# Performance work log

Hardware: AMD Instinct MI355X
Metric: run time of the kernel (lower is better)

The kernel has to match this reference:

```python
import jax, jax.numpy as jnp
import numpy as np
from jax import lax

MARGIN = 0.5
EPS = 1e-12


def _l2norm(x, axis=-1):
    n = jnp.sqrt(jnp.sum(x * x, axis=axis, keepdims=True))
    return x / jnp.maximum(n, EPS)


def setup_inputs() -> dict:
    key = jax.random.key(0)
    ks = jax.random.split(key, 18)
    B, T, N, Din = 1, 8, 4096, 128
    hid = 256
    D = 2 * hid  # out_dim = 2*hidden_dim[-1]
    Tp, Ttr, M, K = 4, 5, 2048, 16
    s = 0.05
    return {
        "x_feature": jax.random.normal(ks[0], (B, Ttr, N, 1), jnp.float32),
        "x_graph": jax.random.normal(ks[1], (B, T, N, Din), jnp.float32),
        "x_graph_inv": jax.random.normal(ks[2], (B, T, N, Din), jnp.float32),
        "temp_y": jax.random.randint(ks[3], (Tp, M, 2 + K), 0, N),
        "is_leaf": jax.random.uniform(ks[4], (Tp, N), dtype=jnp.float32),
        "W_gcn": jax.random.normal(ks[5], (Din, hid), jnp.float32) * s,
        "b_gcn": jnp.zeros((hid,), jnp.float32),
        "Wx_zr": jax.random.normal(ks[6], (D, 2 * D), jnp.float32) * s,
        "Wh_zr": jax.random.normal(ks[7], (D, 2 * D), jnp.float32) * s,
        "b_zr": jnp.zeros((2 * D,), jnp.float32),
        "Wx_c": jax.random.normal(ks[8], (D, D), jnp.float32) * s,
        "Wh_c": jax.random.normal(ks[9], (D, D), jnp.float32) * s,
        "b_c": jnp.zeros((D,), jnp.float32),
        "h_vecs": jax.random.normal(ks[10], (Tp, D), jnp.float32),
        "W_leaf": jax.random.normal(ks[11], (D, 1), jnp.float32) * s,
        "b_leaf": jnp.zeros((1,), jnp.float32),
        "W_conv": jax.random.normal(ks[12], (Ttr, Tp), jnp.float32) * s,
        "b_conv": jnp.zeros((Tp,), jnp.float32),
        "cur_node_num": N,
    }


def reference(x_feature, x_graph, x_graph_inv, temp_y, is_leaf,
              W_gcn, b_gcn, Wx_zr, Wh_zr, b_zr, Wx_c, Wh_c, b_c,
              h_vecs, W_leaf, b_leaf, W_conv, b_conv, cur_node_num):
    B = x_graph.shape[0]
    N_all = x_graph.shape[2]
    # t_gcn on both graph views, concat -> [B,T,N,D]
    h = jax.nn.relu(jnp.einsum('btnd,dh->btnh', x_graph, W_gcn) + b_gcn)
    h_inv = jax.nn.relu(jnp.einsum('btnd,dh->btnh', x_graph_inv, W_gcn) + b_gcn)
    h_final = jnp.concatenate((h, h_inv), axis=-1)
    D = h_final.shape[-1]

    # sequential GRU (TGCNCell) over time_span via scan
    def cell(hs, x):
        zr = jax.nn.sigmoid(x @ Wx_zr + hs @ Wh_zr + b_zr)
        z, r = jnp.split(zr, 2, axis=-1)
        c = jnp.tanh(x @ Wx_c + (r * hs) @ Wh_c + b_c)
        return z * hs + (1.0 - z) * c, None

    h0 = jnp.zeros((B, N_all, D), h_final.dtype)
    hT, _ = lax.scan(cell, h0, jnp.moveaxis(h_final, 1, 0))
    h_trans = _l2norm(hT.reshape(-1, D)[:cur_node_num])  # [N,D]

    # grid predictions (t_conv surrogate): [B,Ttr,N,1] -> [Tp, B*N] -> [Tp,N]
    feat = x_feature[..., 0].transpose(0, 2, 1)            # [B,N,Ttr]
    g = feat @ W_conv + b_conv                             # [B,N,Tp]
    grid_x = jnp.moveaxis(g, 2, 0).reshape(g.shape[-1], -1)[:, :cur_node_num]

    # Householder reflections per predicted step
    hn = _l2norm(h_vecs)                                   # [Tp,D]
    W_trans = jnp.eye(D, dtype=hn.dtype) - 2.0 * hn[:, :, None] * hn[:, None, :]

    leaf_logits = jax.nn.sigmoid(h_trans @ W_leaf + b_leaf)  # [N,1]
    lvec = leaf_logits[:, 0]

    def per_t(W_t, idx_t, yleaf_t, grid_t):
        pos = h_trans[idx_t[:, 1]]            # [M,D]
        neg = h_trans[idx_t[:, 2:]]           # [M,K,D]
        a = pos @ W_t                          # [M,D]
        score_neg = 1.0 - jnp.einsum('md,mkd->mk', a, neg)
        score_pos = 1.0 - jnp.sum(a * pos, axis=-1, keepdims=True)
        loss_off = jnp.mean(jax.nn.relu(score_pos - score_neg + MARGIN))
        # BCEWithLogits applied to sigmoid outputs (faithful to source)
        loss_leaf = jnp.mean(jnp.maximum(lvec, 0.0) - lvec * yleaf_t + jnp.log1p(jnp.exp(-jnp.abs(lvec))))
        h_s = h_trans @ W_t                    # [N,D]
        score_all = h_s @ h_s.T                # [N,N]
        final = lvec * grid_t                  # [N]
        att = score_all @ final                # [N]
        return att, loss_off, loss_leaf

    att_pre, lo, ll = jax.vmap(per_t)(W_trans, temp_y, is_leaf, grid_x)
    return att_pre, jnp.mean(lo), jnp.mean(ll)
```

## Files before the change

### kernel.cpp

```cpp
#include <hip/hip_runtime.h>
#include <hip/hip_bf16.h>
#include <hip/hip_fp16.h>
#include <math.h>

typedef __hip_bfloat16 bf16;
typedef __attribute__((ext_vector_type(8))) short short8;
typedef __attribute__((ext_vector_type(4))) float f32x4;

union UB { short8 v; bf16 e[8]; };
union UH { short8 v; __half e[8]; };

__device__ __forceinline__ float wred(float v) {
  #pragma unroll
  for (int o = 32; o > 0; o >>= 1) v += __shfl_xor(v, o, 64);
  return v;
}
__device__ __forceinline__ float sigf(float x) { return 1.f / (1.f + expf(-x)); }

__device__ __forceinline__ float sig2(float x) {
  return __builtin_amdgcn_rcpf(1.f + exp2f(-1.44269504f * x));
}
__device__ __forceinline__ float tanh2(float x) {
  float ax = fminf(fabsf(x), 30.f);
  float e = exp2f(2.88539008f * ax);
  float r = 1.f - 2.f * __builtin_amdgcn_rcpf(e + 1.f);
  return copysignf(r, x);
}

__device__ __forceinline__ void gl_lds16(const bf16* g, const bf16* lds) {
  __builtin_amdgcn_global_load_lds((const __attribute__((address_space(1))) void*)g,
                                   (__attribute__((address_space(3))) void*)lds,
                                   16, 0, 0);
}
__device__ __forceinline__ void gl_lds16c(const bf16* g, const bf16* lds) {
  __builtin_amdgcn_global_load_lds((const __attribute__((address_space(1))) void*)g,
                                   (__attribute__((address_space(3))) void*)lds,
                                   16, 0, 1);
}
__device__ __forceinline__ f32x4 mfma16(short8 a, short8 b, f32x4 c) {
  return __builtin_amdgcn_mfma_f32_16x16x32_bf16(a, b, c, 0, 0, 0);
}

__device__ __forceinline__ void gang_sync(unsigned* f) {
  __syncthreads();
  if (threadIdx.x == 0) {
    __hip_atomic_fetch_add(f, 1u, __ATOMIC_RELAXED, __HIP_MEMORY_SCOPE_AGENT);
    int it = 0;
    while (__hip_atomic_load(f, __ATOMIC_RELAXED, __HIP_MEMORY_SCOPE_AGENT) < 4u) {
      __builtin_amdgcn_s_sleep(2);
      if (++it > (1 << 27)) break;
    }
  }
  __syncthreads();
  asm volatile("" ::: "memory");
}

__global__ __launch_bounds__(256, 2)
void gemmx(const bf16* __restrict__ A, const bf16* __restrict__ Wxzrt,
           const bf16* __restrict__ Wxct, const float* __restrict__ b_zr,
           const float* __restrict__ b_c, bf16* __restrict__ xzrp,
           bf16* __restrict__ xcp)
{
  __shared__ __align__(16) char smem[34816];
  bf16* As = (bf16*)smem;
  bf16* Bs = (bf16*)(smem + 16384);
  __half* Ts = (__half*)smem;

  const int tid  = threadIdx.x;
  const int wave = tid >> 6, lane = tid & 63;
  const int lm = lane & 15, q = lane >> 4;
  const int brow = blockIdx.x, bcol = blockIdx.y;
  const int wr = (wave >> 1) * 64, wc = (wave & 1) * 64;
  const int srow = lane >> 3, sslot = lane & 7;

  const bf16* Bt; const float* bias; bf16* C; int ldc, colbase;
  if (bcol < 8) { Bt = Wxzrt + (size_t)bcol * 128 * 512; bias = b_zr; C = xzrp; ldc = 1024; colbase = bcol * 128; }
  else          { Bt = Wxct + (size_t)(bcol - 8) * 128 * 512; bias = b_c; C = xcp; ldc = 512; colbase = (bcol - 8) * 128; }

  f32x4 acc[4][4];
  #pragma unroll
  for (int i = 0; i < 4; ++i)
    #pragma unroll
    for (int j = 0; j < 4; ++j) acc[i][j] = (f32x4){0.f, 0.f, 0.f, 0.f};

  for (int kb = 0; kb < 512; kb += 64) {
    #pragma unroll
    for (int j = 0; j < 4; ++j) {
      int ml = wave * 32 + j * 8 + srow;
      int cg = sslot ^ (ml & 7);
      gl_lds16(A + (size_t)(brow * 128 + ml) * 512 + kb + cg * 8, As + (wave * 4 + j) * 512);
      gl_lds16(Bt + (size_t)ml * 512 + kb + cg * 8, Bs + (wave * 4 + j) * 512);
    }
    __syncthreads();
    #pragma unroll
    for (int ks = 0; ks < 2; ++ks) {
      short8 af[4], bfr[4];
      #pragma unroll
      for (int i = 0; i < 4; ++i) {
        int cg = ks * 4 + q;
        int ml = wr + i * 16 + lm;
        af[i]  = *(const short8*)(As + ml * 64 + ((cg ^ (ml & 7)) * 8));
        int nl = wc + i * 16 + lm;
        bfr[i] = *(const short8*)(Bs + nl * 64 + ((cg ^ (nl & 7)) * 8));
      }
      #pragma unroll
      for (int i = 0; i < 4; ++i)
        #pragma unroll
        for (int j = 0; j < 4; ++j)
          acc[i][j] = mfma16(af[i], bfr[j], acc[i][j]);
    }
    __syncthreads();
  }
  #pragma unroll
  for (int i = 0; i < 4; ++i)
    #pragma unroll
    for (int j = 0; j < 4; ++j) {
      int col = wc + j * 16 + lm;
      float bv = bias[colbase + col];
      #pragma unroll
      for (int p = 0; p < 4; ++p)
        Ts[(wr + i * 16 + q * 4 + p) * 136 + col] = __float2half(acc[i][j][p] + bv);
    }
  __syncthreads();
  int rg = tid >> 4, cl = tid & 15;
  #pragma unroll
  for (int v = 0; v < 8; ++v) {
    int row = v * 16 + rg;
    UH t; t.v = *(const short8*)(Ts + row * 136 + cl * 8);
    UB o;
    #pragma unroll
    for (int e = 0; e < 8; ++e) o.e[e] = __float2bfloat16(__half2float(t.e[e]));
    *(short8*)(C + (size_t)(brow * 128 + row) * ldc + colbase + cl * 8) = o.v;
  }
}

__global__ __launch_bounds__(256, 2)
void gcnk(const float* __restrict__ Ag, const float* __restrict__ Agi,
          const bf16* __restrict__ Wgt, const float* __restrict__ bias,
          bf16* __restrict__ out)
{
  __shared__ __align__(16) char smem[34816];
  bf16* As = (bf16*)smem;
  bf16* Bs = (bf16*)(smem + 16384);
  __half* Ts = (__half*)smem;

  const int tid  = threadIdx.x;
  const int wave = tid >> 6, lane = tid & 63;
  const int lm = lane & 15, q = lane >> 4;
  const int brow = blockIdx.x, bcol = blockIdx.y;
  const int z = blockIdx.z, cout = z * 256;
  const float* A = z ? Agi : Ag;
  const int wr = (wave >> 1) * 64, wc = (wave & 1) * 64;
  const int srow = lane >> 3, sslot = lane & 7;

  f32x4 acc[4][4];
  #pragma unroll
  for (int i = 0; i < 4; ++i)
    #pragma unroll
    for (int j = 0; j < 4; ++j) acc[i][j] = (f32x4){0.f, 0.f, 0.f, 0.f};

  for (int kb = 0; kb < 128; kb += 64) {
    #pragma unroll
    for (int j = 0; j < 4; ++j) {
      int ml = wave * 32 + j * 8 + srow;
      int cg = sslot ^ (ml & 7);
      const float* src = A + (size_t)(brow * 128 + ml) * 128 + kb + cg * 8;
      bf16 tmp[8];
      #pragma unroll
      for (int e = 0; e < 8; ++e) tmp[e] = __float2bfloat16(src[e]);
      *(short8*)(As + ml * 64 + sslot * 8) = *(const short8*)tmp;
      gl_lds16(Wgt + (size_t)(bcol * 128 + ml) * 128 + kb + cg * 8,
               Bs + (wave * 4 + j) * 512);
    }
    __syncthreads();
    #pragma unroll
    for (int ks = 0; ks < 2; ++ks) {
      short8 af[4], bfr[4];
      #pragma unroll
      for (int i = 0; i < 4; ++i) {
        int cg = ks * 4 + q;
        int ml = wr + i * 16 + lm;
        af[i]  = *(const short8*)(As + ml * 64 + ((cg ^ (ml & 7)) * 8));
        int nl = wc + i * 16 + lm;
        bfr[i] = *(const short8*)(Bs + nl * 64 + ((cg ^ (nl & 7)) * 8));
      }
      #pragma unroll
      for (int i = 0; i < 4; ++i)
        #pragma unroll
        for (int j = 0; j < 4; ++j)
          acc[i][j] = mfma16(af[i], bfr[j], acc[i][j]);
    }
    __syncthreads();
  }
  #pragma unroll
  for (int i = 0; i < 4; ++i)
    #pragma unroll
    for (int j = 0; j < 4; ++j) {
      int col = wc + j * 16 + lm;
      float bv = bias[bcol * 128 + col];
      #pragma unroll
      for (int p = 0; p < 4; ++p)
        Ts[(wr + i * 16 + q * 4 + p) * 136 + col] = __float2half(acc[i][j][p] + bv);
    }
  __syncthreads();
  int rg = tid >> 4, cl = tid & 15;
  #pragma unroll
  for (int v = 0; v < 8; ++v) {
    int row = v * 16 + rg;
    UH t; t.v = *(const short8*)(Ts + row * 136 + cl * 8);
    UB o;
    #pragma unroll
    for (int e = 0; e < 8; ++e) o.e[e] = __float2bfloat16(fmaxf(__half2float(t.e[e]), 0.f));
    *(short8*)(out + (size_t)(brow * 128 + row) * 512 + cout + bcol * 128 + cl * 8) = o.v;
  }
}

__global__ __launch_bounds__(512, 1)
void grup(const bf16* __restrict__ Wzr, const bf16* __restrict__ Wc,
          const bf16* __restrict__ xzrp, const bf16* __restrict__ xcp,
          bf16* __restrict__ rhb, bf16* __restrict__ hsb,
          unsigned* __restrict__ flags)
{
  __shared__ __align__(16) bf16   As[64 * 512];
  __shared__ __align__(16) __half zs[64 * 128];
  __shared__ __align__(16) bf16   hs[64 * 128];
  __half* Ts = (__half*)As;

  const int tid  = threadIdx.x;
  const int w    = tid >> 6, lane = tid & 63;
  const int lm   = lane & 15, q = lane >> 4;
  const int bid  = blockIdx.x;
  const int s    = (bid >> 3) & 3;
  const int g    = ((bid >> 5) << 3) | (bid & 7);
  const int grow = g * 64;
  const int grp  = w >> 2, wq = w & 3;
  const int rh_  = w & 1, cq = w >> 1;
  const int prow = tid >> 3;
  const size_t gr = (size_t)(grow + prow);
  const int pc1 = (tid & 7) * 32;
  const int pc2 = (tid & 7) * 16;
  unsigned* gf = flags + g * 16;

  for (int t = 0; t < 8; ++t) {
    const bool t0 = (t == 0);
    const bf16* xz = xzrp + (size_t)t * 4096 * 1024;
    const bf16* xc = xcp  + (size_t)t * 4096 * 512;

    {
      const bool zchunk = (pc1 < 128);
      const int zrcol = zchunk ? (s * 128 + pc1) : (512 + s * 128 + pc1 - 128);
      UB xv[4];
      #pragma unroll
      for (int j = 0; j < 4; ++j)
        xv[j].v = *(const short8*)(xz + gr * 1024 + zrcol + j * 8);

      f32x4 acc[4][2];
      #pragma unroll
      for (int mf = 0; mf < 4; ++mf)
        #pragma unroll
        for (int nf = 0; nf < 2; ++nf) acc[mf][nf] = (f32x4){0.f, 0.f, 0.f, 0.f};

      if (!t0) {
        #pragma unroll
        for (int j = 0; j < 8; ++j) {
          int row = w * 8 + j;
          gl_lds16c(hsb + (size_t)(grow + row) * 512 + ((lane ^ (row & 7)) * 8),
                    As + row * 512);
        }
        __syncthreads();

        const int nb0 = (grp ? 32 : 0) + s * 8 + wq * 2;
        const bf16* Bp = Wzr + (size_t)nb0 * 8192 + lane * 8;
        #pragma unroll
        for (int KS = 0; KS < 16; ++KS) {
          short8 a[4], b[2];
          #pragma unroll
          for (int mf = 0; mf < 4; ++mf) {
            int row = mf * 16 + lm;
            a[mf] = *(const short8*)(As + row * 512 + (((KS * 4 + q) ^ (row & 7)) * 8));
          }
          #pragma unroll
          for (int nf = 0; nf < 2; ++nf)
            b[nf] = *(const short8*)(Bp + (size_t)nf * 8192 + KS * 512);
          #pragma unroll
          for (int nf = 0; nf < 2; ++nf)
            #pragma unroll
            for (int mf = 0; mf < 4; ++mf)
              acc[mf][nf] = mfma16(a[mf], b[nf], acc[mf][nf]);
        }
        __syncthreads();
      }

      #pragma unroll
      for (int mf = 0; mf < 4; ++mf)
        #pragma unroll
        for (int nf = 0; nf < 2; ++nf)
          #pragma unroll
          for (int p = 0; p < 4; ++p)
            Ts[(mf * 16 + q * 4 + p) * 264 + w * 32 + nf * 16 + lm] =
              __float2half(acc[mf][nf][p]);
      __syncthreads();

      #pragma unroll
      for (int j = 0; j < 4; ++j) {
        int c = pc1 + j * 8;
        UH tv; tv.v = *(const short8*)(Ts + prow * 264 + c);
        if (zchunk) {
          UH o;
          #pragma unroll
          for (int e = 0; e < 8; ++e)
            o.e[e] = __float2half(sig2(__half2float(tv.e[e]) + (float)xv[j].e[e]));
          *(short8*)(zs + prow * 128 + c) = o.v;
        } else if (!t0) {
          UB h8; h8.v = *(const short8*)(hs + prow * 128 + (c - 128));
          UB o;
          #pragma unroll
          for (int e = 0; e < 8; ++e) {
            float r = sig2(__half2float(tv.e[e]) + (float)xv[j].e[e]);
            o.e[e] = __float2bfloat16(r * (float)h8.e[e]);
          }
          *(short8*)(rhb + gr * 512 + s * 128 + (c - 128)) = o.v;
        }
      }
    }
    gang_sync(gf + 2 * t);

    {
      UB xv[2];
      #pragma unroll
      for (int j = 0; j < 2; ++j)
        xv[j].v = *(const short8*)(xc + gr * 512 + s * 128 + pc2 + j * 8);

      f32x4 acc[2][2];
      #pragma unroll
      for (int mf = 0; mf < 2; ++mf)
        #pragma unroll
        for (int nf = 0; nf < 2; ++nf) acc[mf][nf] = (f32x4){0.f, 0.f, 0.f, 0.f};

      if (!t0) {
        #pragma unroll
        for (int j = 0; j < 8; ++j) {
          int row = w * 8 + j;
          gl_lds16c(rhb + (size_t)(grow + row) * 512 + ((lane ^ (row & 7)) * 8),
                    As + row * 512);
        }
        __syncthreads();

        const bf16* Bp = Wc + (size_t)(s * 8 + cq * 2) * 8192 + lane * 8;
        #pragma unroll
        for (int KS = 0; KS < 16; ++KS) {
          short8 a[2], b[2];
          #pragma unroll
          for (int mf = 0; mf < 2; ++mf) {
            int row = rh_ * 32 + mf * 16 + lm;
            a[mf] = *(const short8*)(As + row * 512 + (((KS * 4 + q) ^ (row & 7)) * 8));
          }
          #pragma unroll
          for (int nf = 0; nf < 2; ++nf)
            b[nf] = *(const short8*)(Bp + (size_t)nf * 8192 + KS * 512);
          #pragma unroll
          for (int nf = 0; nf < 2; ++nf)
            #pragma unroll
            for (int mf = 0; mf < 2; ++mf)
              acc[mf][nf] = mfma16(a[mf], b[nf], acc[mf][nf]);
        }
        __syncthreads();
      }

      #pragma unroll
      for (int mf = 0; mf < 2; ++mf)
        #pragma unroll
        for (int nf = 0; nf < 2; ++nf)
          #pragma unroll
          for (int p = 0; p < 4; ++p)
            Ts[(rh_ * 32 + mf * 16 + q * 4 + p) * 136 + cq * 32 + nf * 16 + lm] =
              __float2half(acc[mf][nf][p]);
      __syncthreads();

      #pragma unroll
      for (int j = 0; j < 2; ++j) {
        int c = pc2 + j * 8;
        UH tv; tv.v = *(const short8*)(Ts + prow * 136 + c);
        UH zv; zv.v = *(const short8*)(zs + prow * 128 + c);
        UB h8;
        if (!t0) h8.v = *(const short8*)(hs + prow * 128 + c);
        UB o;
        #pragma unroll
        for (int e = 0; e < 8; ++e) {
          float cd = tanh2(__half2float(tv.e[e]) + (float)xv[j].e[e]);
          float zc = __half2float(zv.e[e]);
          float ho = t0 ? 0.f : (float)h8.e[e];
          o.e[e] = __float2bfloat16(zc * ho + (1.f - zc) * cd);
        }
        *(short8*)(hs + prow * 128 + c) = o.v;
        *(short8*)(hsb + gr * 512 + s * 128 + c) = o.v;
      }
    }
    if (t < 7) gang_sync(gf + 2 * t + 1);
  }
}

__global__ void prep(const float* __restrict__ Wh_zr, const float* __restrict__ Wh_c,
                     const float* __restrict__ Wx_zr, const float* __restrict__ Wx_c,
                     const float* __restrict__ W_gcn,
                     bf16* __restrict__ Whzrt, bf16* __restrict__ Whct,
                     bf16* __restrict__ Wxzrt, bf16* __restrict__ Wxct,
                     bf16* __restrict__ Wgt) {
  int i = blockIdx.x * 256 + threadIdx.x;
  if (i < 524288) {
    int n = i >> 9, k = i & 511;
    int off = ((n >> 4) * 16 + (k >> 5)) * 512 + ((k >> 3) & 3) * 128 + (n & 15) * 8 + (k & 7);
    Whzrt[off] = __float2bfloat16(Wh_zr[(size_t)k * 1024 + n]);
  } else if (i < 786432) {
    int j = i - 524288; int n = j >> 9, k = j & 511;
    int off = ((n >> 4) * 16 + (k >> 5)) * 512 + ((k >> 3) & 3) * 128 + (n & 15) * 8 + (k & 7);
    Whct[off] = __float2bfloat16(Wh_c[(size_t)k * 512 + n]);
  } else if (i < 1310720) {
    int j = i - 786432; int n = j >> 9, k = j & 511;
    Wxzrt[j] = __float2bfloat16(Wx_zr[(size_t)k * 1024 + n]);
  } else if (i < 1572864) {
    int j = i - 1310720; int n = j >> 9, k = j & 511;
    Wxct[j] = __float2bfloat16(Wx_c[(size_t)k * 512 + n]);
  } else {
    int j = i - 1572864; int n = j >> 7, k = j & 127;
    Wgt[j] = __float2bfloat16(W_gcn[(size_t)k * 256 + n]);
  }
}

__global__ void norm_lvec(const bf16* __restrict__ hsb, const float* __restrict__ Wl,
                          const float* __restrict__ bl, const float* __restrict__ hv,
                          bf16* __restrict__ Htrb, float* __restrict__ lv,
                          float* __restrict__ hn) {
  int w = threadIdx.x >> 6, lane = threadIdx.x & 63;
  if (blockIdx.x == 1024) {
    float x[8], ss = 0.f;
    #pragma unroll
    for (int j = 0; j < 8; ++j) { x[j] = hv[w * 512 + lane * 8 + j]; ss += x[j] * x[j]; }
    ss = wred(ss);
    float inv = 1.f / fmaxf(sqrtf(ss), 1e-12f);
    #pragma unroll
    for (int j = 0; j < 8; ++j) hn[w * 512 + lane * 8 + j] = x[j] * inv;
    return;
  }
  int n = blockIdx.x * 4 + w;
  float x[8], ss = 0.f;
  #pragma unroll
  for (int j = 0; j < 8; ++j) {
    x[j] = (float)hsb[(size_t)n * 512 + lane * 8 + j];
    ss += x[j] * x[j];
  }
  ss = wred(ss);
  float inv = 1.f / fmaxf(sqrtf(ss), 1e-12f);
  float dot = 0.f;
  #pragma unroll
  for (int j = 0; j < 8; ++j) {
    float vv = x[j] * inv;
    Htrb[(size_t)n * 512 + lane * 8 + j] = __float2bfloat16(vv);
    dot += vv * Wl[lane * 8 + j];
  }
  dot = wred(dot);
  if (lane == 0) lv[n] = sigf(dot + bl[0]);
}

__global__ void htf(const bf16* __restrict__ Htrb, const float* __restrict__ xf,
                    const float* __restrict__ Wc, const float* __restrict__ bc,
                    const float* __restrict__ lv, float* __restrict__ v) {
  __shared__ float fin_s[4][64];
  int ch = blockIdx.x;
  int d = threadIdx.x;
  int n0 = ch * 64;
  if (d < 256) {
    int t = d >> 6, i = d & 63, n = n0 + i;
    float g = bc[t];
    #pragma unroll
    for (int tt = 0; tt < 5; ++tt) g += xf[tt * 4096 + n] * Wc[tt * 4 + t];
    fin_s[t][i] = lv[n] * g;
  }
  __syncthreads();
  float s0 = 0.f, s1 = 0.f, s2 = 0.f, s3 = 0.f;
  for (int i = 0; i < 64; ++i) {
    float hv = (float)Htrb[(size_t)(n0 + i) * 512 + d];
    s0 += hv * fin_s[0][i];
    s1 += hv * fin_s[1][i];
    s2 += hv * fin_s[2][i];
    s3 += hv * fin_s[3][i];
  }
  atomicAdd(&v[d], s0);
  atomicAdd(&v[512 + d], s1);
  atomicAdd(&v[1024 + d], s2);
  atomicAdd(&v[1536 + d], s3);
}

__global__ void attk(const bf16* __restrict__ Htrb, const float* __restrict__ v,
                     float* __restrict__ out) {
  int w = threadIdx.x >> 6, lane = threadIdx.x & 63;
  int n = blockIdx.x * 4 + w;
  float x[8];
  #pragma unroll
  for (int j = 0; j < 8; ++j) x[j] = (float)Htrb[(size_t)n * 512 + lane * 8 + j];
  #pragma unroll
  for (int t = 0; t < 4; ++t) {
    float s = 0.f;
    #pragma unroll
    for (int j = 0; j < 8; ++j) s += x[j] * v[t * 512 + lane * 8 + j];
    s = wred(s);
    if (lane == 0) out[t * 4096 + n] = s;
  }
}

__global__ void loff(const bf16* __restrict__ Htrb, const float* __restrict__ hn,
                     const int* __restrict__ ty, float* __restrict__ loffp) {
  int w = threadIdx.x >> 6, lane = threadIdx.x & 63;
  int t = blockIdx.y;
  int m = blockIdx.x * 4 + w;
  const int* row = ty + ((size_t)t * 2048 + m) * 18;
  int pi = row[1];
  float p[8], hv[8], c = 0.f;
  #pragma unroll
  for (int j = 0; j < 8; ++j) {
    p[j]  = (float)Htrb[(size_t)pi * 512 + lane * 8 + j];
    hv[j] = hn[t * 512 + lane * 8 + j];
    c += p[j] * hv[j];
  }
  c = wred(c);
  float a[8], sp = 0.f;
  #pragma unroll
  for (int j = 0; j < 8; ++j) { a[j] = p[j] - 2.f * c * hv[j]; sp += a[j] * p[j]; }
  sp = wred(sp);
  float acc = 0.f;
  for (int k = 0; k < 16; ++k) {
    int ni = row[2 + k];
    float sn = 0.f;
    #pragma unroll
    for (int j = 0; j < 8; ++j) sn += a[j] * (float)Htrb[(size_t)ni * 512 + lane * 8 + j];
    sn = wred(sn);
    acc += fmaxf(sn - sp + 0.5f, 0.f);
  }
  __shared__ float sbuf[4];
  if (lane == 0) sbuf[w] = acc;
  __syncthreads();
  if (threadIdx.x == 0)
    loffp[t * 512 + blockIdx.x] = sbuf[0] + sbuf[1] + sbuf[2] + sbuf[3];
}

__global__ void fini(const float* __restrict__ loffp, const float* __restrict__ lv,
                     const float* __restrict__ yl, float* __restrict__ out) {
  int tid = threadIdx.x, w = tid >> 6, lane = tid & 63;
  float s = 0.f, s2 = 0.f;
  for (int i = tid; i < 2048; i += 256) s += loffp[i];
  for (int i = tid; i < 4096; i += 256) {
    float l = lv[i];
    float ym = 0.25f * (yl[i] + yl[4096 + i] + yl[8192 + i] + yl[12288 + i]);
    s2 += fmaxf(l, 0.f) - l * ym + log1pf(expf(-fabsf(l)));
  }
  s = wred(s); s2 = wred(s2);
  __shared__ float sb[4], sb2[4];
  if (lane == 0) { sb[w] = s; sb2[w] = s2; }
  __syncthreads();
  if (tid == 0) {
    out[16384] = (sb[0] + sb[1] + sb[2] + sb[3]) / (4.f * 2048.f * 16.f);
    out[16385] = (sb2[0] + sb2[1] + sb2[2] + sb2[3]) / 4096.f;
  }
}

__global__ void wsprobe(float marker, float* out) {
  if (threadIdx.x == 0) out[0] = marker;
}

extern "C" void kernel_launch(void* const* d_in, const int* in_sizes, int n_in,
                              void* d_out, int out_size, void* d_ws, size_t ws_size,
                              hipStream_t stream) {
  const float* x_feature   = (const float*)d_in[0];
  const float* x_graph     = (const float*)d_in[1];
  const float* x_graph_inv = (const float*)d_in[2];
  const int*   temp_y      = (const int*)d_in[3];
  const float* is_leaf     = (const float*)d_in[4];
  const float* W_gcn       = (const float*)d_in[5];
  const float* b_gcn       = (const float*)d_in[6];
  const float* Wx_zr       = (const float*)d_in[7];
  const float* Wh_zr       = (const float*)d_in[8];
  const float* b_zr        = (const float*)d_in[9];
  const float* Wx_c        = (const float*)d_in[10];
  const float* Wh_c        = (const float*)d_in[11];
  const float* b_c         = (const float*)d_in[12];
  const float* h_vecs      = (const float*)d_in[13];
  const float* W_leaf      = (const float*)d_in[14];
  const float* b_leaf      = (const float*)d_in[15];
  const float* W_conv      = (const float*)d_in[16];
  const float* b_conv      = (const float*)d_in[17];
  float* out = (float*)d_out;
  (void)in_sizes; (void)n_in; (void)out_size;

  const size_t NEED = 156000000;
  if (ws_size < NEED) {
    wsprobe<<<1, 64, 0, stream>>>(1000.f + (float)(ws_size >> 20), out);
    return;
  }

  char* ws = (char*)d_ws;
  size_t off = 0;
  auto alloc = [&](size_t bytes) -> void* {
    void* p = ws + off;
    off = (off + bytes + 255) & ~(size_t)255;
    return p;
  };
  bf16*   Whzrt = (bf16*)  alloc((size_t)1024 * 512 * 2);
  bf16*   Whct  = (bf16*)  alloc((size_t)512 * 512 * 2);
  bf16*   Wxzrt = (bf16*)  alloc((size_t)1024 * 512 * 2);
  bf16*   Wxct  = (bf16*)  alloc((size_t)512 * 512 * 2);
  bf16*   Wgt   = (bf16*)  alloc((size_t)256 * 128 * 2);
  bf16*   hfin  = (bf16*)  alloc((size_t)32768 * 512 * 2);
  bf16*   xzrp  = (bf16*)  alloc((size_t)32768 * 1024 * 2);
  bf16*   xcp   = (bf16*)  alloc((size_t)32768 * 512 * 2);
  bf16*   hsb   = (bf16*)  alloc((size_t)4096 * 512 * 2);
  bf16*   rhb   = (bf16*)  alloc((size_t)4096 * 512 * 2);
  float*  lv    = (float*) alloc(4096 * 4);
  float*  hn    = (float*) alloc(4 * 512 * 4);
  float*  v     = (float*) alloc(4 * 512 * 4);
  float*  loffp = (float*) alloc(2048 * 4);
  unsigned* flags = (unsigned*)alloc(64 * 16 * 4);
  bf16*   Htrb  = hfin;

  hipMemsetAsync(v, 0, 4 * 512 * 4, stream);
  hipMemsetAsync(flags, 0, 64 * 16 * 4, stream);

  prep<<<6272, 256, 0, stream>>>(Wh_zr, Wh_c, Wx_zr, Wx_c, W_gcn,
                                 Whzrt, Whct, Wxzrt, Wxct, Wgt);
  gcnk<<<dim3(256, 2, 2), 256, 0, stream>>>(x_graph, x_graph_inv, Wgt, b_gcn, hfin);
  gemmx<<<dim3(256, 12), 256, 0, stream>>>(hfin, Wxzrt, Wxct, b_zr, b_c, xzrp, xcp);

  grup<<<256, 512, 0, stream>>>(Whzrt, Whct, xzrp, xcp, rhb, hsb, flags);

  norm_lvec<<<1025, 256, 0, stream>>>(hsb, W_leaf, b_leaf, h_vecs, Htrb, lv, hn);
  htf<<<64, 512, 0, stream>>>(Htrb, x_feature, W_conv, b_conv, lv, v);
  attk<<<1024, 256, 0, stream>>>(Htrb, v, out);
  loff<<<dim3(512, 4), 256, 0, stream>>>(Htrb, hn, temp_y, loffp);
  fini<<<1, 256, 0, stream>>>(loffp, lv, is_leaf, out);
}
```

Before: 448.4 us.

## Fuse input-projection GEMM into persistent GRU kernel, dropping xzrp/xcp buffers

Removes the separate gemmx kernel that precomputed x@Wx_zr and x@Wx_c for all timesteps into large bf16 buffers. The persistent GRU kernel now loads each timestep's hfin rows into a new shared-memory tile and does the input-projection MFMAs alongside the hidden-state ones, with biases folded into the accumulator initialisation. This saves the intermediate writes and reads and one launch. In exchange it puts more MFMA work and shared memory on the serial recurrent critical path, where only 256 blocks run.

New measurement: 665.7 us. 48.5% more time.

```diff
diff --git a/kernel.cpp b/kernel.cpp
--- a/kernel.cpp
+++ b/kernel.cpp
@@ -56,85 +56,6 @@
 }
 
 __global__ __launch_bounds__(256, 2)
-void gemmx(const bf16* __restrict__ A, const bf16* __restrict__ Wxzrt,
-           const bf16* __restrict__ Wxct, const float* __restrict__ b_zr,
-           const float* __restrict__ b_c, bf16* __restrict__ xzrp,
-           bf16* __restrict__ xcp)
-{
-  __shared__ __align__(16) char smem[34816];
-  bf16* As = (bf16*)smem;
-  bf16* Bs = (bf16*)(smem + 16384);
-  __half* Ts = (__half*)smem;
-
-  const int tid  = threadIdx.x;
-  const int wave = tid >> 6, lane = tid & 63;
-  const int lm = lane & 15, q = lane >> 4;
-  const int brow = blockIdx.x, bcol = blockIdx.y;
-  const int wr = (wave >> 1) * 64, wc = (wave & 1) * 64;
-  const int srow = lane >> 3, sslot = lane & 7;
-
-  const bf16* Bt; const float* bias; bf16* C; int ldc, colbase;
-  if (bcol < 8) { Bt = Wxzrt + (size_t)bcol * 128 * 512; bias = b_zr; C = xzrp; ldc = 1024; colbase = bcol * 128; }
-  else          { Bt = Wxct + (size_t)(bcol - 8) * 128 * 512; bias = b_c; C = xcp; ldc = 512; colbase = (bcol - 8) * 128; }
-
-  f32x4 acc[4][4];
-  #pragma unroll
-  for (int i = 0; i < 4; ++i)
-    #pragma unroll
-    for (int j = 0; j < 4; ++j) acc[i][j] = (f32x4){0.f, 0.f, 0.f, 0.f};
-
-  for (int kb = 0; kb < 512; kb += 64) {
-    #pragma unroll
-    for (int j = 0; j < 4; ++j) {
-      int ml = wave * 32 + j * 8 + srow;
-      int cg = sslot ^ (ml & 7);
-      gl_lds16(A + (size_t)(brow * 128 + ml) * 512 + kb + cg * 8, As + (wave * 4 + j) * 512);
-      gl_lds16(Bt + (size_t)ml * 512 + kb + cg * 8, Bs + (wave * 4 + j) * 512);
-    }
-    __syncthreads();
-    #pragma unroll
-    for (int ks = 0; ks < 2; ++ks) {
-      short8 af[4], bfr[4];
-      #pragma unroll
-      for (int i = 0; i < 4; ++i) {
-        int cg = ks * 4 + q;
-        int ml = wr + i * 16 + lm;
-        af[i]  = *(const short8*)(As + ml * 64 + ((cg ^ (ml & 7)) * 8));
-        int nl = wc + i * 16 + lm;
-        bfr[i] = *(const short8*)(Bs + nl * 64 + ((cg ^ (nl & 7)) * 8));
-      }
-      #pragma unroll
-      for (int i = 0; i < 4; ++i)
-        #pragma unroll
-        for (int j = 0; j < 4; ++j)
-          acc[i][j] = mfma16(af[i], bfr[j], acc[i][j]);
-    }
-    __syncthreads();
-  }
-  #pragma unroll
-  for (int i = 0; i < 4; ++i)
-    #pragma unroll
-    for (int j = 0; j < 4; ++j) {
-      int col = wc + j * 16 + lm;
-      float bv = bias[colbase + col];
-      #pragma unroll
-      for (int p = 0; p < 4; ++p)
-        Ts[(wr + i * 16 + q * 4 + p) * 136 + col] = __float2half(acc[i][j][p] + bv);
-    }
-  __syncthreads();
-  int rg = tid >> 4, cl = tid & 15;
-  #pragma unroll
-  for (int v = 0; v < 8; ++v) {
-    int row = v * 16 + rg;
-    UH t; t.v = *(const short8*)(Ts + row * 136 + cl * 8);
-    UB o;
-    #pragma unroll
-    for (int e = 0; e < 8; ++e) o.e[e] = __float2bfloat16(__half2float(t.e[e]));
-    *(short8*)(C + (size_t)(brow * 128 + row) * ldc + colbase + cl * 8) = o.v;
-  }
-}
-
-__global__ __launch_bounds__(256, 2)
 void gcnk(const float* __restrict__ Ag, const float* __restrict__ Agi,
           const bf16* __restrict__ Wgt, const float* __restrict__ bias,
           bf16* __restrict__ out)
@@ -217,11 +138,13 @@
 
 __global__ __launch_bounds__(512, 1)
 void grup(const bf16* __restrict__ Wzr, const bf16* __restrict__ Wc,
-          const bf16* __restrict__ xzrp, const bf16* __restrict__ xcp,
-          bf16* __restrict__ rhb, bf16* __restrict__ hsb,
-          unsigned* __restrict__ flags)
+          const bf16* __restrict__ Wxzr, const bf16* __restrict__ Wxc,
+          const bf16* __restrict__ hfin, const float* __restrict__ bzr,
+          const float* __restrict__ bc, bf16* __restrict__ rhb,
+          bf16* __restrict__ hsb, unsigned* __restrict__ flags)
 {
   __shared__ __align__(16) bf16   As[64 * 512];
+  __shared__ __align__(16) bf16   Xs[64 * 512];
   __shared__ __align__(16) __half zs[64 * 128];
   __shared__ __align__(16) bf16   hs[64 * 128];
   __half* Ts = (__half*)As;
@@ -243,23 +166,15 @@
 
   for (int t = 0; t < 8; ++t) {
     const bool t0 = (t == 0);
-    const bf16* xz = xzrp + (size_t)t * 4096 * 1024;
-    const bf16* xc = xcp  + (size_t)t * 4096 * 512;
 
     {
-      const bool zchunk = (pc1 < 128);
-      const int zrcol = zchunk ? (s * 128 + pc1) : (512 + s * 128 + pc1 - 128);
-      UB xv[4];
-      #pragma unroll
-      for (int j = 0; j < 4; ++j)
-        xv[j].v = *(const short8*)(xz + gr * 1024 + zrcol + j * 8);
-
-      f32x4 acc[4][2];
-      #pragma unroll
-      for (int mf = 0; mf < 4; ++mf)
-        #pragma unroll
-        for (int nf = 0; nf < 2; ++nf) acc[mf][nf] = (f32x4){0.f, 0.f, 0.f, 0.f};
-
+      const bf16* xsrc = hfin + ((size_t)(t * 4096) + grow) * 512;
+      #pragma unroll
+      for (int j = 0; j < 8; ++j) {
+        int row = w * 8 + j;
+        gl_lds16(xsrc + (size_t)row * 512 + ((lane ^ (row & 7)) * 8),
+                 Xs + row * 512);
+      }
       if (!t0) {
         #pragma unroll
         for (int j = 0; j < 8; ++j) {
@@ -267,9 +182,20 @@
           gl_lds16c(hsb + (size_t)(grow + row) * 512 + ((lane ^ (row & 7)) * 8),
                     As + row * 512);
         }
-        __syncthreads();
-
-        const int nb0 = (grp ? 32 : 0) + s * 8 + wq * 2;
+      }
+      __syncthreads();
+
+      const int nb0 = (grp ? 32 : 0) + s * 8 + wq * 2;
+      f32x4 acc[4][2];
+      #pragma unroll
+      for (int nf = 0; nf < 2; ++nf) {
+        float bv = bzr[(nb0 + nf) * 16 + lm];
+        #pragma unroll
+        for (int mf = 0; mf < 4; ++mf)
+          acc[mf][nf] = (f32x4){bv, bv, bv, bv};
+      }
+
+      if (!t0) {
         const bf16* Bp = Wzr + (size_t)nb0 * 8192 + lane * 8;
         #pragma unroll
         for (int KS = 0; KS < 16; ++KS) {
@@ -288,8 +214,28 @@
             for (int mf = 0; mf < 4; ++mf)
               acc[mf][nf] = mfma16(a[mf], b[nf], acc[mf][nf]);
         }
-        __syncthreads();
-      }
+      }
+      {
+        const bf16* Bp = Wxzr + (size_t)nb0 * 8192 + lane * 8;
+        #pragma unroll
+        for (int KS = 0; KS < 16; ++KS) {
+          short8 a[4], b[2];
+          #pragma unroll
+          for (int mf = 0; mf < 4; ++mf) {
+            int row = mf * 16 + lm;
+            a[mf] = *(const short8*)(Xs + row * 512 + (((KS * 4 + q) ^ (row & 7)) * 8));
+          }
+          #pragma unroll
+          for (int nf = 0; nf < 2; ++nf)
+            b[nf] = *(const short8*)(Bp + (size_t)nf * 8192 + KS * 512);
+          #pragma unroll
+          for (int nf = 0; nf < 2; ++nf)
+            #pragma unroll
+            for (int mf = 0; mf < 4; ++mf)
+              acc[mf][nf] = mfma16(a[mf], b[nf], acc[mf][nf]);
+        }
+      }
+      __syncthreads();
 
       #pragma unroll
       for (int mf = 0; mf < 4; ++mf)
@@ -305,18 +251,18 @@
       for (int j = 0; j < 4; ++j) {
         int c = pc1 + j * 8;
         UH tv; tv.v = *(const short8*)(Ts + prow * 264 + c);
-        if (zchunk) {
+        if (c < 128) {
           UH o;
           #pragma unroll
           for (int e = 0; e < 8; ++e)
-            o.e[e] = __float2half(sig2(__half2float(tv.e[e]) + (float)xv[j].e[e]));
+            o.e[e] = __float2half(sig2(__half2float(tv.e[e])));
           *(short8*)(zs + prow * 128 + c) = o.v;
         } else if (!t0) {
           UB h8; h8.v = *(const short8*)(hs + prow * 128 + (c - 128));
           UB o;
           #pragma unroll
           for (int e = 0; e < 8; ++e) {
-            float r = sig2(__half2float(tv.e[e]) + (float)xv[j].e[e]);
+            float r = sig2(__half2float(tv.e[e]));
             o.e[e] = __float2bfloat16(r * (float)h8.e[e]);
           }
           *(short8*)(rhb + gr * 512 + s * 128 + (c - 128)) = o.v;
@@ -326,17 +272,6 @@
     gang_sync(gf + 2 * t);
 
     {
-      UB xv[2];
-      #pragma unroll
-      for (int j = 0; j < 2; ++j)
-        xv[j].v = *(const short8*)(xc + gr * 512 + s * 128 + pc2 + j * 8);
-
-      f32x4 acc[2][2];
-      #pragma unroll
-      for (int mf = 0; mf < 2; ++mf)
-        #pragma unroll
-        for (int nf = 0; nf < 2; ++nf) acc[mf][nf] = (f32x4){0.f, 0.f, 0.f, 0.f};
-
       if (!t0) {
         #pragma unroll
         for (int j = 0; j < 8; ++j) {
@@ -344,9 +279,21 @@
           gl_lds16c(rhb + (size_t)(grow + row) * 512 + ((lane ^ (row & 7)) * 8),
                     As + row * 512);
         }
-        __syncthreads();
-
-        const bf16* Bp = Wc + (size_t)(s * 8 + cq * 2) * 8192 + lane * 8;
+      }
+      __syncthreads();
+
+      const int nb2 = s * 8 + cq * 2;
+      f32x4 acc[2][2];
+      #pragma unroll
+      for (int nf = 0; nf < 2; ++nf) {
+        float bv = bc[(nb2 + nf) * 16 + lm];
+        #pragma unroll
+        for (int mf = 0; mf < 2; ++mf)
+          acc[mf][nf] = (f32x4){bv, bv, bv, bv};
+      }
+
+      if (!t0) {
+        const bf16* Bp = Wc + (size_t)nb2 * 8192 + lane * 8;
         #pragma unroll
         for (int KS = 0; KS < 16; ++KS) {
           short8 a[2], b[2];
@@ -364,8 +311,28 @@
             for (int mf = 0; mf < 2; ++mf)
               acc[mf][nf] = mfma16(a[mf], b[nf], acc[mf][nf]);
         }
-        __syncthreads();
-      }
+      }
+      {
+        const bf16* Bp = Wxc + (size_t)nb2 * 8192 + lane * 8;
+        #pragma unroll
+        for (int KS = 0; KS < 16; ++KS) {
+          short8 a[2], b[2];
+          #pragma unroll
+          for (int mf = 0; mf < 2; ++mf) {
+            int row = rh_ * 32 + mf * 16 + lm;
+            a[mf] = *(const short8*)(Xs + row * 512 + (((KS * 4 + q) ^ (row & 7)) * 8));
+          }
+          #pragma unroll
+          for (int nf = 0; nf < 2; ++nf)
+            b[nf] = *(const short8*)(Bp + (size_t)nf * 8192 + KS * 512);
+          #pragma unroll
+          for (int nf = 0; nf < 2; ++nf)
+            #pragma unroll
+            for (int mf = 0; mf < 2; ++mf)
+              acc[mf][nf] = mfma16(a[mf], b[nf], acc[mf][nf]);
+        }
+      }
+      __syncthreads();
 
       #pragma unroll
       for (int mf = 0; mf < 2; ++mf)
@@ -387,7 +354,7 @@
         UB o;
         #pragma unroll
         for (int e = 0; e < 8; ++e) {
-          float cd = tanh2(__half2float(tv.e[e]) + (float)xv[j].e[e]);
+          float cd = tanh2(__half2float(tv.e[e]));
           float zc = __half2float(zv.e[e]);
           float ho = t0 ? 0.f : (float)h8.e[e];
           o.e[e] = __float2bfloat16(zc * ho + (1.f - zc) * cd);
@@ -417,10 +384,12 @@
     Whct[off] = __float2bfloat16(Wh_c[(size_t)k * 512 + n]);
   } else if (i < 1310720) {
     int j = i - 786432; int n = j >> 9, k = j & 511;
-    Wxzrt[j] = __float2bfloat16(Wx_zr[(size_t)k * 1024 + n]);
+    int off = ((n >> 4) * 16 + (k >> 5)) * 512 + ((k >> 3) & 3) * 128 + (n & 15) * 8 + (k & 7);
+    Wxzrt[off] = __float2bfloat16(Wx_zr[(size_t)k * 1024 + n]);
   } else if (i < 1572864) {
     int j = i - 1310720; int n = j >> 9, k = j & 511;
-    Wxct[j] = __float2bfloat16(Wx_c[(size_t)k * 512 + n]);
+    int off = ((n >> 4) * 16 + (k >> 5)) * 512 + ((k >> 3) & 3) * 128 + (n & 15) * 8 + (k & 7);
+    Wxct[off] = __float2bfloat16(Wx_c[(size_t)k * 512 + n]);
   } else {
     int j = i - 1572864; int n = j >> 7, k = j & 127;
     Wgt[j] = __float2bfloat16(W_gcn[(size_t)k * 256 + n]);
@@ -591,7 +560,7 @@
   float* out = (float*)d_out;
   (void)in_sizes; (void)n_in; (void)out_size;
 
-  const size_t NEED = 156000000;
+  const size_t NEED = 60000000;
   if (ws_size < NEED) {
     wsprobe<<<1, 64, 0, stream>>>(1000.f + (float)(ws_size >> 20), out);
     return;
@@ -610,8 +579,6 @@
   bf16*   Wxct  = (bf16*)  alloc((size_t)512 * 512 * 2);
   bf16*   Wgt   = (bf16*)  alloc((size_t)256 * 128 * 2);
   bf16*   hfin  = (bf16*)  alloc((size_t)32768 * 512 * 2);
-  bf16*   xzrp  = (bf16*)  alloc((size_t)32768 * 1024 * 2);
-  bf16*   xcp   = (bf16*)  alloc((size_t)32768 * 512 * 2);
   bf16*   hsb   = (bf16*)  alloc((size_t)4096 * 512 * 2);
   bf16*   rhb   = (bf16*)  alloc((size_t)4096 * 512 * 2);
   float*  lv    = (float*) alloc(4096 * 4);
@@ -627,9 +594,9 @@
   prep<<<6272, 256, 0, stream>>>(Wh_zr, Wh_c, Wx_zr, Wx_c, W_gcn,
                                  Whzrt, Whct, Wxzrt, Wxct, Wgt);
   gcnk<<<dim3(256, 2, 2), 256, 0, stream>>>(x_graph, x_graph_inv, Wgt, b_gcn, hfin);
-  gemmx<<<dim3(256, 12), 256, 0, stream>>>(hfin, Wxzrt, Wxct, b_zr, b_c, xzrp, xcp);
-
-  grup<<<256, 512, 0, stream>>>(Whzrt, Whct, xzrp, xcp, rhb, hsb, flags);
+
+  grup<<<256, 512, 0, stream>>>(Whzrt, Whct, Wxzrt, Wxct, hfin,
+                                b_zr, b_c, rhb, hsb, flags);
 
   norm_lvec<<<1025, 256, 0, stream>>>(hsb, W_leaf, b_leaf, h_vecs, Htrb, lv, hn);
   htf<<<64, 512, 0, stream>>>(Htrb, x_feature, W_conv, b_conv, lv, v);
```
